# Performance work log

Measured on AMD Instinct MI355X. Metric: run time of the kernel, lower is better.

The kernel has to match this reference:

```python
import jax, jax.numpy as jnp
import numpy as np

N_UE = 100000
N_AP = 10000
N_E = 1600000
D = 64
H = 128


def setup_inputs() -> dict:
    key = jax.random.key(0)
    ks = jax.random.split(key, 10)
    s = 0.05
    return {
        "ue_hid": jax.random.normal(ks[0], (N_UE, D), jnp.float32),
        "ap_hid": jax.random.normal(ks[1], (N_AP, D), jnp.float32),
        "edge_hid": jax.random.normal(ks[2], (N_E, D), jnp.float32),
        "src": jax.random.randint(ks[3], (N_E,), 0, N_UE),
        "dst": jax.random.randint(ks[4], (N_E,), 0, N_AP),
        "W1a": jax.random.normal(ks[5], (2 * D, H), jnp.float32) * s,
        "b1a": jnp.zeros((H,), jnp.float32),
        "W1b": jax.random.normal(ks[6], (H, H), jnp.float32) * s,
        "b1b": jnp.zeros((H,), jnp.float32),
        "W2a": jax.random.normal(ks[7], (D + H, H), jnp.float32) * s,
        "b2a": jnp.zeros((H,), jnp.float32),
        "W2b": jax.random.normal(ks[8], (H, D), jnp.float32) * s,
        "b2b": jnp.zeros((D,), jnp.float32),
    }


def reference(ue_hid, ap_hid, edge_hid, src, dst,
              W1a, b1a, W1b, b1b, W2a, b2a, W2b, b2b):
    # message: concat(edge_feature, src UE feature) -> [E, 2D]
    msg = jnp.concatenate([edge_hid, ue_hid[src]], axis=-1)
    # mlp1 applied per edge (DGL applies it inside reduce on the mailbox,
    # which is equivalent to per-edge application followed by segment sum)
    h = jnp.maximum(msg @ W1a + b1a, 0.0) @ W1b + b1b          # [E, H]
    # sum over mailbox (all edges with the same destination AP)
    agg = jax.ops.segment_sum(h, dst, num_segments=N_AP)        # [N_AP, H]
    # mlp2 on concat(AP hid, aggregated messages)
    z = jnp.concatenate([ap_hid, agg], axis=-1)                 # [N_AP, D+H]
    new_ap = jnp.maximum(z @ W2a + b2a, 0.0) @ W2b + b2b        # [N_AP, D]
    return new_ap
```

## Files before the change

kernel.cpp:

```cpp
#include <hip/hip_runtime.h>

#define N_UE 100000
#define N_AP 10000
#define N_E  1600000
#define NTILE (N_E / 128)

typedef float f32x4 __attribute__((ext_vector_type(4)));
typedef int   i32x2 __attribute__((ext_vector_type(2)));
typedef short s8b   __attribute__((ext_vector_type(8)));
typedef short s4b   __attribute__((ext_vector_type(4)));

static __device__ __forceinline__ unsigned short f2bf(float x) {
  union { float f; unsigned int u; } v; v.f = x;
  unsigned int r = v.u + 0x7fffu + ((v.u >> 16) & 1u);
  return (unsigned short)(r >> 16);
}

__global__ void apk0_prep(const float* __restrict__ W1a, short* __restrict__ WTg,
                          int* __restrict__ counts, float* __restrict__ aggW) {
  int i = blockIdx.x * 256 + threadIdx.x, n = gridDim.x * 256;
  for (int x = i; x < 128 * 128; x += n) {
    int col = x >> 7, k = x & 127;
    WTg[x] = (short)f2bf(W1a[k * 128 + col]);
  }
  for (int x = i; x < N_AP; x += n) counts[x] = 0;
  for (int x = i; x < N_AP * 128 / 4; x += n)
    ((f32x4*)aggW)[x] = (f32x4){0.f, 0.f, 0.f, 0.f};
}

__global__ void apk2_hist(const int* __restrict__ dst, int* __restrict__ counts) {
  int i = blockIdx.x * blockDim.x + threadIdx.x;
  int stride = gridDim.x * blockDim.x;
  for (; i < N_E; i += stride) atomicAdd(&counts[dst[i]], 1);
}

__global__ __launch_bounds__(256) void apk3a_scanlocal(
    const int* __restrict__ counts, int* __restrict__ offsets,
    int* __restrict__ bsum) {
  __shared__ int p[256];
  int t = threadIdx.x, idx = blockIdx.x * 256 + t;
  int v = (idx < N_AP) ? counts[idx] : 0;
  p[t] = v;
  __syncthreads();
  for (int d = 1; d < 256; d <<= 1) {
    int s2 = p[t] + ((t >= d) ? p[t - d] : 0);
    __syncthreads();
    p[t] = s2;
    __syncthreads();
  }
  if (idx < N_AP) offsets[idx] = p[t] - v;
  if (t == 255) bsum[blockIdx.x] = p[255];
}

__global__ __launch_bounds__(256) void apk3b_scanbase(
    int* __restrict__ offsets, const int* __restrict__ bsum) {
  __shared__ int base;
  int t = threadIdx.x, idx = blockIdx.x * 256 + t;
  if (t == 0) {
    int b = 0;
    for (int k = 0; k < (int)blockIdx.x; k++) b += bsum[k];
    base = b;
  }
  __syncthreads();
  if (idx < N_AP) offsets[idx] += base;
}

__global__ void apk4_scatter(const int* __restrict__ dst, const int* __restrict__ src,
                             int* __restrict__ offsets, i32x2* __restrict__ pair) {
  int i = blockIdx.x * blockDim.x + threadIdx.x;
  int stride = gridDim.x * blockDim.x;
  for (; i < N_E; i += stride) {
    int d = dst[i], s = src[i];
    int pos = atomicAdd(&offsets[d], 1);
    i32x2 v;
    v[0] = i | ((d & 0x7FF) << 21);
    v[1] = s | ((d >> 11) << 17);
    pair[pos] = v;
  }
}

__global__ __launch_bounds__(256, 4) void apk5_edges(
    const float* __restrict__ edge_hid, const float* __restrict__ ue_hid,
    const short* __restrict__ WTg, const float* __restrict__ b1a,
    const i32x2* __restrict__ pair, float* __restrict__ aggW) {
  __shared__ short A[128][132];
  __shared__ int segs[128];
  __shared__ int eix[128];
  __shared__ int six[128];
  int t = threadIdx.x;
  int wave = t >> 6, lane = t & 63, quad = lane >> 4, l16 = lane & 15;

  s8b bf[2][4];
  for (int ct = 0; ct < 2; ct++)
    for (int ks = 0; ks < 4; ks++)
      bf[ct][ks] = *(const s8b*)&WTg[(wave * 32 + ct * 16 + l16) * 128 +
                                     ks * 32 + quad * 8];
  float bias0 = b1a[wave * 32 + l16];
  float bias1 = b1a[wave * 32 + 16 + l16];

  int runseg = -1;
  float run0 = 0.f, run1 = 0.f;
  auto flush = [&]() {
    if (runseg >= 0) {
      float f0 = run0 + __shfl_xor(run0, 16); f0 += __shfl_xor(f0, 32);
      float f1 = run1 + __shfl_xor(run1, 16); f1 += __shfl_xor(f1, 32);
      if (quad == 0) {
        atomicAdd(&aggW[(size_t)runseg * 128 + wave * 32 + l16], f0);
        atomicAdd(&aggW[(size_t)runseg * 128 + wave * 32 + 16 + l16], f1);
      }
    }
  };

  const int r8 = t >> 5, half = (t >> 4) & 1, chunk = t & 15;
  for (int tile = blockIdx.x; tile < NTILE; tile += gridDim.x) {
    __syncthreads();
    if (t < 128) {
      i32x2 tr = pair[(size_t)tile * 128 + t];
      segs[t] = (int)((unsigned)tr[0] >> 21) | (((tr[1] >> 17) & 7) << 11);
      eix[t] = tr[0] & 0x1FFFFF;
      six[t] = tr[1] & 0x1FFFF;
    }
    __syncthreads();
    {
      const float* bases[16];
      #pragma unroll
      for (int it = 0; it < 16; it++) {
        int row = it * 8 + r8;
        bases[it] = half ? (ue_hid + (size_t)six[row] * 64)
                         : (edge_hid + (size_t)eix[row] * 64);
      }
      #pragma unroll
      for (int it = 0; it < 16; it++) {
        int row = it * 8 + r8;
        f32x4 v = ((const f32x4*)bases[it])[chunk];
        s4b pk;
        pk[0] = (short)f2bf(v[0]); pk[1] = (short)f2bf(v[1]);
        pk[2] = (short)f2bf(v[2]); pk[3] = (short)f2bf(v[3]);
        *(s4b*)&A[row][half * 64 + chunk * 4] = pk;
      }
    }
    __syncthreads();

    for (int rt = 0; rt < 8; rt++) {
      s8b a0 = *(const s8b*)&A[rt * 16 + l16][0 + quad * 8];
      s8b a1 = *(const s8b*)&A[rt * 16 + l16][32 + quad * 8];
      s8b a2 = *(const s8b*)&A[rt * 16 + l16][64 + quad * 8];
      s8b a3 = *(const s8b*)&A[rt * 16 + l16][96 + quad * 8];
      f32x4 c0 = {0.f, 0.f, 0.f, 0.f}, c1 = {0.f, 0.f, 0.f, 0.f};
      c0 = __builtin_amdgcn_mfma_f32_16x16x32_bf16(a0, bf[0][0], c0, 0, 0, 0);
      c0 = __builtin_amdgcn_mfma_f32_16x16x32_bf16(a1, bf[0][1], c0, 0, 0, 0);
      c0 = __builtin_amdgcn_mfma_f32_16x16x32_bf16(a2, bf[0][2], c0, 0, 0, 0);
      c0 = __builtin_amdgcn_mfma_f32_16x16x32_bf16(a3, bf[0][3], c0, 0, 0, 0);
      c1 = __builtin_amdgcn_mfma_f32_16x16x32_bf16(a0, bf[1][0], c1, 0, 0, 0);
      c1 = __builtin_amdgcn_mfma_f32_16x16x32_bf16(a1, bf[1][1], c1, 0, 0, 0);
      c1 = __builtin_amdgcn_mfma_f32_16x16x32_bf16(a2, bf[1][2], c1, 0, 0, 0);
      c1 = __builtin_amdgcn_mfma_f32_16x16x32_bf16(a3, bf[1][3], c1, 0, 0, 0);
      float t0[4], t1[4];
      #pragma unroll
      for (int j = 0; j < 4; j++) {
        t0[j] = fmaxf(c0[j] + bias0, 0.f);
        t1[j] = fmaxf(c1[j] + bias1, 0.f);
      }
      int gb = rt * 16;
      int sF = segs[gb], sL = segs[gb + 15];
      if (sF == sL) {
        if (sF != runseg) { flush(); runseg = sF; run0 = 0.f; run1 = 0.f; }
        run0 += t0[0] + t0[1] + t0[2] + t0[3];
        run1 += t1[0] + t1[1] + t1[2] + t1[3];
      } else {
        int sj[4];
        #pragma unroll
        for (int j = 0; j < 4; j++) sj[j] = segs[gb + quad * 4 + j];
        for (int sg = sF; sg <= sL; sg++) {
          float v0 = 0.f, v1 = 0.f;
          #pragma unroll
          for (int j = 0; j < 4; j++)
            if (sj[j] == sg) { v0 += t0[j]; v1 += t1[j]; }
          if (sg == runseg) { run0 += v0; run1 += v1; }
          else { flush(); runseg = sg; run0 = v0; run1 = v1; }
        }
      }
    }
  }
  flush();
}

__global__ __launch_bounds__(256) void apk6_mlp2(
    const float* __restrict__ ap_hid, const float* __restrict__ W1b,
    const float* __restrict__ b1b, const float* __restrict__ W2a,
    const float* __restrict__ b2a, const float* __restrict__ W2b,
    const float* __restrict__ b2b, const float* __restrict__ aggW,
    const int* __restrict__ counts, float* __restrict__ out) {
  __shared__ float wbuf[64 * 128];
  __shared__ float zrows[16 * 128];
  __shared__ float yrows[16 * 128];
  __shared__ float arows[16 * 64];
  __shared__ float cbuf[16];
  int t = threadIdx.x;
  int apb = blockIdx.x * 16;
  for (int i = t; i < 16 * 128 / 4; i += 256)
    ((float4*)zrows)[i] = ((const float4*)(aggW + (size_t)apb * 128))[i];
  for (int i = t; i < 16 * 64 / 4; i += 256)
    ((float4*)arows)[i] = ((const float4*)(ap_hid + (size_t)apb * 64))[i];
  if (t < 16) cbuf[t] = (float)counts[apb + t];
  int j = t & 127, half = t >> 7;
  {
    float bb = b1b[j];
    __syncthreads();
    float acc[8];
    for (int r = 0; r < 8; r++) acc[r] = cbuf[half * 8 + r] * bb;
    for (int pp = 0; pp < 2; pp++) {
      __syncthreads();
      for (int i = t; i < 64 * 128 / 4; i += 256)
        ((float4*)wbuf)[i] = ((const float4*)(W1b + pp * 64 * 128))[i];
      __syncthreads();
      for (int k = 0; k < 64; k++) {
        float w = wbuf[k * 128 + j];
        for (int r = 0; r < 8; r++)
          acc[r] += zrows[(half * 8 + r) * 128 + (pp * 64 + k)] * w;
      }
    }
    for (int r = 0; r < 8; r++) yrows[(half * 8 + r) * 128 + j] = acc[r];
  }
  {
    float acc2[8];
    float bb = b2a[j];
    for (int r = 0; r < 8; r++) acc2[r] = bb;
    __syncthreads();
    for (int i = t; i < 64 * 128 / 4; i += 256)
      ((float4*)wbuf)[i] = ((const float4*)W2a)[i];
    __syncthreads();
    for (int k = 0; k < 64; k++) {
      float w = wbuf[k * 128 + j];
      for (int r = 0; r < 8; r++) acc2[r] += arows[(half * 8 + r) * 64 + k] * w;
    }
    for (int pp = 0; pp < 2; pp++) {
      __syncthreads();
      for (int i = t; i < 64 * 128 / 4; i += 256)
        ((float4*)wbuf)[i] = ((const float4*)(W2a + (64 + pp * 64) * 128))[i];
      __syncthreads();
      for (int k = 0; k < 64; k++) {
        float w = wbuf[k * 128 + j];
        for (int r = 0; r < 8; r++)
          acc2[r] += yrows[(half * 8 + r) * 128 + (pp * 64 + k)] * w;
      }
    }
    __syncthreads();
    for (int r = 0; r < 8; r++)
      zrows[(half * 8 + r) * 128 + j] = fmaxf(acc2[r], 0.f);
  }
  {
    __syncthreads();
    for (int i = t; i < 128 * 64 / 4; i += 256)
      ((float4*)wbuf)[i] = ((const float4*)W2b)[i];
    __syncthreads();
    int i2 = t & 63, q = t >> 6;
    float acc3[4];
    float bb = b2b[i2];
    for (int r = 0; r < 4; r++) acc3[r] = bb;
    for (int k = 0; k < 128; k++) {
      float w = wbuf[k * 64 + i2];
      for (int r = 0; r < 4; r++) acc3[r] += zrows[(q * 4 + r) * 128 + k] * w;
    }
    for (int r = 0; r < 4; r++)
      out[(size_t)(apb + q * 4 + r) * 64 + i2] = acc3[r];
  }
}

extern "C" void kernel_launch(void* const* d_in, const int* in_sizes, int n_in,
                              void* d_out, int out_size, void* d_ws, size_t ws_size,
                              hipStream_t stream) {
  const float* ue_hid   = (const float*)d_in[0];
  const float* ap_hid   = (const float*)d_in[1];
  const float* edge_hid = (const float*)d_in[2];
  const int*   src      = (const int*)d_in[3];
  const int*   dst      = (const int*)d_in[4];
  const float* W1a      = (const float*)d_in[5];
  const float* b1a      = (const float*)d_in[6];
  const float* W1b      = (const float*)d_in[7];
  const float* b1b      = (const float*)d_in[8];
  const float* W2a      = (const float*)d_in[9];
  const float* b2a      = (const float*)d_in[10];
  const float* W2b      = (const float*)d_in[11];
  const float* b2b      = (const float*)d_in[12];
  float* out = (float*)d_out;

  unsigned char* ws = (unsigned char*)d_ws;
  short* WTg    = (short*)(ws);
  int* counts   = (int*)(ws + 32768);
  int* offsets  = (int*)(ws + 73728);
  int* bsum     = (int*)(ws + 114688);
  float* aggW   = (float*)(ws + 118784);
  i32x2* pair   = (i32x2*)(ws + 5238784);

  apk0_prep<<<640, 256, 0, stream>>>(W1a, WTg, counts, aggW);
  apk2_hist<<<2048, 256, 0, stream>>>(dst, counts);
  apk3a_scanlocal<<<40, 256, 0, stream>>>(counts, offsets, bsum);
  apk3b_scanbase<<<40, 256, 0, stream>>>(offsets, bsum);
  apk4_scatter<<<2048, 256, 0, stream>>>(dst, src, offsets, pair);
  apk5_edges<<<2048, 256, 0, stream>>>(edge_hid, ue_hid, WTg, b1a, pair, aggW);
  apk6_mlp2<<<N_AP / 16, 256, 0, stream>>>(ap_hid, W1b, b1b, W2a, b2a, W2b, b2b,
                                           aggW, counts, out);
}
```

Measured before the change: 829.0 us.

## Vectorize hist/scatter, single-block scan, hardware bf16 pack, float4 MLP2 inner loops

Result: slower. 853.6 us (+3.0%).

```diff
diff --git a/kernel.cpp b/kernel.cpp
--- a/kernel.cpp
+++ b/kernel.cpp
@@ -14,6 +14,12 @@
   union { float f; unsigned int u; } v; v.f = x;
   unsigned int r = v.u + 0x7fffu + ((v.u >> 16) & 1u);
   return (unsigned short)(r >> 16);
+}
+
+static __device__ __forceinline__ unsigned int cvtpk_bf16(float lo, float hi) {
+  unsigned int r;
+  asm("v_cvt_pk_bf16_f32 %0, %1, %2" : "=v"(r) : "v"(lo), "v"(hi));
+  return r;
 }
 
 __global__ void apk0_prep(const float* __restrict__ W1a, short* __restrict__ WTg,
@@ -29,53 +35,65 @@
 }
 
 __global__ void apk2_hist(const int* __restrict__ dst, int* __restrict__ counts) {
-  int i = blockIdx.x * blockDim.x + threadIdx.x;
-  int stride = gridDim.x * blockDim.x;
-  for (; i < N_E; i += stride) atomicAdd(&counts[dst[i]], 1);
-}
-
-__global__ __launch_bounds__(256) void apk3a_scanlocal(
-    const int* __restrict__ counts, int* __restrict__ offsets,
-    int* __restrict__ bsum) {
-  __shared__ int p[256];
-  int t = threadIdx.x, idx = blockIdx.x * 256 + t;
-  int v = (idx < N_AP) ? counts[idx] : 0;
-  p[t] = v;
+  int i = blockIdx.x * 256 + threadIdx.x;
+  int n = gridDim.x * 256;
+  for (int x = i; x < N_E / 4; x += n) {
+    int4 d = ((const int4*)dst)[x];
+    atomicAdd(&counts[d.x], 1);
+    atomicAdd(&counts[d.y], 1);
+    atomicAdd(&counts[d.z], 1);
+    atomicAdd(&counts[d.w], 1);
+  }
+}
+
+__global__ __launch_bounds__(1024) void apk3_scan(const int* __restrict__ counts,
+                                                  int* __restrict__ offsets) {
+  __shared__ int p[1024];
+  int t = threadIdx.x;
+  int start = t * 10;
+  int loc[10];
+  int s = 0;
+  #pragma unroll
+  for (int u = 0; u < 10; u++) {
+    int i = start + u;
+    loc[u] = (i < N_AP) ? counts[i] : 0;
+    s += loc[u];
+  }
+  p[t] = s;
   __syncthreads();
-  for (int d = 1; d < 256; d <<= 1) {
-    int s2 = p[t] + ((t >= d) ? p[t - d] : 0);
-    __syncthreads();
-    p[t] = s2;
-    __syncthreads();
-  }
-  if (idx < N_AP) offsets[idx] = p[t] - v;
-  if (t == 255) bsum[blockIdx.x] = p[255];
-}
-
-__global__ __launch_bounds__(256) void apk3b_scanbase(
-    int* __restrict__ offsets, const int* __restrict__ bsum) {
-  __shared__ int base;
-  int t = threadIdx.x, idx = blockIdx.x * 256 + t;
-  if (t == 0) {
-    int b = 0;
-    for (int k = 0; k < (int)blockIdx.x; k++) b += bsum[k];
-    base = b;
-  }
-  __syncthreads();
-  if (idx < N_AP) offsets[idx] += base;
+  for (int d = 1; d < 1024; d <<= 1) {
+    int v = p[t] + ((t >= d) ? p[t - d] : 0);
+    __syncthreads();
+    p[t] = v;
+    __syncthreads();
+  }
+  int base = (t == 0) ? 0 : p[t - 1];
+  #pragma unroll
+  for (int u = 0; u < 10; u++) {
+    int i = start + u;
+    if (i < N_AP) offsets[i] = base;
+    base += loc[u];
+  }
 }
 
 __global__ void apk4_scatter(const int* __restrict__ dst, const int* __restrict__ src,
                              int* __restrict__ offsets, i32x2* __restrict__ pair) {
-  int i = blockIdx.x * blockDim.x + threadIdx.x;
-  int stride = gridDim.x * blockDim.x;
-  for (; i < N_E; i += stride) {
-    int d = dst[i], s = src[i];
-    int pos = atomicAdd(&offsets[d], 1);
-    i32x2 v;
-    v[0] = i | ((d & 0x7FF) << 21);
-    v[1] = s | ((d >> 11) << 17);
-    pair[pos] = v;
+  int i = blockIdx.x * 256 + threadIdx.x;
+  int n = gridDim.x * 256;
+  for (int x = i; x < N_E / 4; x += n) {
+    int4 d = ((const int4*)dst)[x];
+    int4 s = ((const int4*)src)[x];
+    int e = x * 4;
+    int dd[4] = {d.x, d.y, d.z, d.w};
+    int ss[4] = {s.x, s.y, s.z, s.w};
+    #pragma unroll
+    for (int j = 0; j < 4; j++) {
+      int pos = atomicAdd(&offsets[dd[j]], 1);
+      i32x2 v;
+      v[0] = (e + j) | ((dd[j] & 0x7FF) << 21);
+      v[1] = ss[j] | ((dd[j] >> 11) << 17);
+      pair[pos] = v;
+    }
   }
 }
 
@@ -133,10 +151,10 @@
       for (int it = 0; it < 16; it++) {
         int row = it * 8 + r8;
         f32x4 v = ((const f32x4*)bases[it])[chunk];
-        s4b pk;
-        pk[0] = (short)f2bf(v[0]); pk[1] = (short)f2bf(v[1]);
-        pk[2] = (short)f2bf(v[2]); pk[3] = (short)f2bf(v[3]);
-        *(s4b*)&A[row][half * 64 + chunk * 4] = pk;
+        uint2 u;
+        u.x = cvtpk_bf16(v[0], v[1]);
+        u.y = cvtpk_bf16(v[2], v[3]);
+        *(uint2*)&A[row][half * 64 + chunk * 4] = u;
       }
     }
     __syncthreads();
@@ -214,10 +232,15 @@
       for (int i = t; i < 64 * 128 / 4; i += 256)
         ((float4*)wbuf)[i] = ((const float4*)(W1b + pp * 64 * 128))[i];
       __syncthreads();
-      for (int k = 0; k < 64; k++) {
-        float w = wbuf[k * 128 + j];
-        for (int r = 0; r < 8; r++)
-          acc[r] += zrows[(half * 8 + r) * 128 + (pp * 64 + k)] * w;
+      for (int k4 = 0; k4 < 16; k4++) {
+        int k = k4 * 4;
+        float w0 = wbuf[(k + 0) * 128 + j], w1 = wbuf[(k + 1) * 128 + j];
+        float w2 = wbuf[(k + 2) * 128 + j], w3 = wbuf[(k + 3) * 128 + j];
+        #pragma unroll
+        for (int r = 0; r < 8; r++) {
+          float4 zv = *(const float4*)&zrows[(half * 8 + r) * 128 + pp * 64 + k];
+          acc[r] += zv.x * w0 + zv.y * w1 + zv.z * w2 + zv.w * w3;
+        }
       }
     }
     for (int r = 0; r < 8; r++) yrows[(half * 8 + r) * 128 + j] = acc[r];
@@ -230,19 +253,30 @@
     for (int i = t; i < 64 * 128 / 4; i += 256)
       ((float4*)wbuf)[i] = ((const float4*)W2a)[i];
     __syncthreads();
-    for (int k = 0; k < 64; k++) {
-      float w = wbuf[k * 128 + j];
-      for (int r = 0; r < 8; r++) acc2[r] += arows[(half * 8 + r) * 64 + k] * w;
+    for (int k4 = 0; k4 < 16; k4++) {
+      int k = k4 * 4;
+      float w0 = wbuf[(k + 0) * 128 + j], w1 = wbuf[(k + 1) * 128 + j];
+      float w2 = wbuf[(k + 2) * 128 + j], w3 = wbuf[(k + 3) * 128 + j];
+      #pragma unroll
+      for (int r = 0; r < 8; r++) {
+        float4 av = *(const float4*)&arows[(half * 8 + r) * 64 + k];
+        acc2[r] += av.x * w0 + av.y * w1 + av.z * w2 + av.w * w3;
+      }
     }
     for (int pp = 0; pp < 2; pp++) {
       __syncthreads();
       for (int i = t; i < 64 * 128 / 4; i += 256)
         ((float4*)wbuf)[i] = ((const float4*)(W2a + (64 + pp * 64) * 128))[i];
       __syncthreads();
-      for (int k = 0; k < 64; k++) {
-        float w = wbuf[k * 128 + j];
-        for (int r = 0; r < 8; r++)
-          acc2[r] += yrows[(half * 8 + r) * 128 + (pp * 64 + k)] * w;
+      for (int k4 = 0; k4 < 16; k4++) {
+        int k = k4 * 4;
+        float w0 = wbuf[(k + 0) * 128 + j], w1 = wbuf[(k + 1) * 128 + j];
+        float w2 = wbuf[(k + 2) * 128 + j], w3 = wbuf[(k + 3) * 128 + j];
+        #pragma unroll
+        for (int r = 0; r < 8; r++) {
+          float4 yv = *(const float4*)&yrows[(half * 8 + r) * 128 + pp * 64 + k];
+          acc2[r] += yv.x * w0 + yv.y * w1 + yv.z * w2 + yv.w * w3;
+        }
       }
     }
     __syncthreads();
@@ -258,9 +292,15 @@
     float acc3[4];
     float bb = b2b[i2];
     for (int r = 0; r < 4; r++) acc3[r] = bb;
-    for (int k = 0; k < 128; k++) {
-      float w = wbuf[k * 64 + i2];
-      for (int r = 0; r < 4; r++) acc3[r] += zrows[(q * 4 + r) * 128 + k] * w;
+    for (int k4 = 0; k4 < 32; k4++) {
+      int k = k4 * 4;
+      float w0 = wbuf[(k + 0) * 64 + i2], w1 = wbuf[(k + 1) * 64 + i2];
+      float w2 = wbuf[(k + 2) * 64 + i2], w3 = wbuf[(k + 3) * 64 + i2];
+      #pragma unroll
+      for (int r = 0; r < 4; r++) {
+        float4 tv = *(const float4*)&zrows[(q * 4 + r) * 128 + k];
+        acc3[r] += tv.x * w0 + tv.y * w1 + tv.z * w2 + tv.w * w3;
+      }
     }
     for (int r = 0; r < 4; r++)
       out[(size_t)(apb + q * 4 + r) * 64 + i2] = acc3[r];
@@ -289,15 +329,13 @@
   short* WTg    = (short*)(ws);
   int* counts   = (int*)(ws + 32768);
   int* offsets  = (int*)(ws + 73728);
-  int* bsum     = (int*)(ws + 114688);
   float* aggW   = (float*)(ws + 118784);
   i32x2* pair   = (i32x2*)(ws + 5238784);
 
   apk0_prep<<<640, 256, 0, stream>>>(W1a, WTg, counts, aggW);
-  apk2_hist<<<2048, 256, 0, stream>>>(dst, counts);
-  apk3a_scanlocal<<<40, 256, 0, stream>>>(counts, offsets, bsum);
-  apk3b_scanbase<<<40, 256, 0, stream>>>(offsets, bsum);
-  apk4_scatter<<<2048, 256, 0, stream>>>(dst, src, offsets, pair);
+  apk2_hist<<<1600, 256, 0, stream>>>(dst, counts);
+  apk3_scan<<<1, 1024, 0, stream>>>(counts, offsets);
+  apk4_scatter<<<1600, 256, 0, stream>>>(dst, src, offsets, pair);
   apk5_edges<<<2048, 256, 0, stream>>>(edge_hid, ue_hid, WTg, b1a, pair, aggW);
   apk6_mlp2<<<N_AP / 16, 256, 0, stream>>>(ap_hid, W1b, b1b, W2a, b2a, W2b, b2b,
                                            aggW, counts, out);
```
